# Kernel tuning notes

Measured on AMD Instinct MI355X. Metric: run time of the kernel, lower is better.

The kernel has to match this reference:

```python
import jax, jax.numpy as jnp
import numpy as np

N = 384          # nodes per graph
HID = 128        # hid_dim
H = 8            # shared_num_heads
C = HID // H     # shared_head_dim = 16
L = 4            # num_layers
VOCAB = 20
NORB = 4
NCAT = NORB * NORB + NORB   # 20 edge categories
OUT = 10
B = 4
E = N * N        # fully-connected closure incl. self loops
EPS = 1e-5


def layer_norm(x, g, b):
    m = jnp.mean(x, axis=-1, keepdims=True)
    v = jnp.mean((x - m) ** 2, axis=-1, keepdims=True)
    return (x - m) / jnp.sqrt(v + EPS) * g + b


def setup_inputs() -> dict:
    key = jax.random.key(0)
    ks = iter(jax.random.split(key, 32))

    def nrm(shape, s=0.05):
        return jax.random.normal(next(ks), shape, jnp.float32) * s

    # edge structure: fully connected, edge (i,j) in row-major order
    pos = np.arange(N) % NORB                    # node -> orbit
    src = np.repeat(np.arange(N), N)
    tgt = np.tile(np.arange(N), N)
    cat = np.where(src == tgt, NORB * NORB + pos[src], pos[src] * NORB + pos[tgt])

    x = jax.random.randint(next(ks), (B, N, 1), 0, VOCAB, jnp.int32)

    return dict(
        x=x,
        edge_src=jnp.asarray(src, jnp.int32),
        edge_tgt=jnp.asarray(tgt, jnp.int32),
        edge_cat=jnp.asarray(cat, jnp.int32),
        token_emb=nrm((VOCAB, HID), 1.0),
        edge_emb=nrm((NCAT, HID), 1.0),
        ln_in1_g=jnp.ones((HID,), jnp.float32), ln_in1_b=jnp.zeros((HID,), jnp.float32),
        W_in=nrm((HID, HID)), b_in=jnp.zeros((HID,), jnp.float32),
        ln_in2_g=jnp.ones((HID,), jnp.float32), ln_in2_b=jnp.zeros((HID,), jnp.float32),
        Wl=nrm((L, HID, H * C)), bl=jnp.zeros((L, H * C), jnp.float32),
        Wr=nrm((L, HID, H * C)), br=jnp.zeros((L, H * C), jnp.float32),
        We=nrm((L, HID, H * C)),                           # lin_edge has no bias in PyG GATv2Conv
        att=nrm((L, H, C)),
        bias_gat=jnp.zeros((L, H * C), jnp.float32),
        W_proj=nrm((L, HID, HID)), b_proj=jnp.zeros((L, HID), jnp.float32),
        ln_g=jnp.ones((L, HID), jnp.float32), ln_b=jnp.zeros((L, HID), jnp.float32),
        W_out=nrm((HID, OUT)), b_out=jnp.zeros((OUT,), jnp.float32),
    )


def reference(x, edge_src, edge_tgt, edge_cat,
              token_emb, edge_emb,
              ln_in1_g, ln_in1_b, W_in, b_in, ln_in2_g, ln_in2_b,
              Wl, bl, Wr, br, We, att, bias_gat,
              W_proj, b_proj, ln_g, ln_b, W_out, b_out):
    edge_feat = edge_emb[edge_cat]                       # [E, HID] gather by category
    h = token_emb[x[..., 0]]                             # [B, N, HID]
    # input MLP: LN -> ReLU -> Linear -> LN
    h = layer_norm(h, ln_in1_g, ln_in1_b)
    h = jax.nn.relu(h)
    h = h @ W_in + b_in
    h = layer_norm(h, ln_in2_g, ln_in2_b)

    for l in range(L):
        edge_e = (edge_feat @ We[l]).reshape(E, H, C)    # shared across batch

        def conv(hb):  # hb: [N, HID]  GATv2Conv, concat heads
            xl = (hb @ Wl[l] + bl[l]).reshape(N, H, C)   # source transform
            xr = (hb @ Wr[l] + br[l]).reshape(N, H, C)   # target transform
            e = jax.nn.leaky_relu(xl[edge_src] + xr[edge_tgt] + edge_e, 0.2)  # [E,H,C]
            logits = jnp.einsum('ehc,hc->eh', e, att[l])                      # [E,H]
            # segment softmax over edges sharing a target node
            m = jax.ops.segment_max(logits, edge_tgt, num_segments=N)
            ex = jnp.exp(logits - m[edge_tgt])
            den = jax.ops.segment_sum(ex, edge_tgt, num_segments=N)
            alpha = ex / den[edge_tgt]                                        # [E,H]
            out = jax.ops.segment_sum(xl[edge_src] * alpha[:, :, None], edge_tgt,
                                      num_segments=N)                         # [N,H,C]
            return out.reshape(N, H * C) + bias_gat[l]

        h_prev = h
        h = jax.vmap(conv)(h)                            # [B, N, HID]
        h = h @ W_proj[l] + b_proj[l]
        h = layer_norm(h, ln_g[l], ln_b[l])
        h = jax.nn.relu(h) + h_prev                      # residual

    h = h.sum(axis=1)                                    # sum over nodes -> [B, HID]
    return h @ W_out + b_out                             # [B, OUT]
```

## Files before the change

kernel.cpp:

```cpp
#include <hip/hip_runtime.h>


#define NN 384
#define NB 4
#define TJ 3

__device__ __forceinline__ void reduce32(float& a, float& b) {
#pragma unroll
  for (int m = 1; m <= 16; m <<= 1) {
    a += __shfl_xor(a, m, 64);
    b += __shfl_xor(b, m, 64);
  }
}

__global__ __launch_bounds__(256) void k_init(
    const int* __restrict__ x,
    const float* __restrict__ token_emb, const float* __restrict__ edge_emb,
    const float* __restrict__ ln1g, const float* __restrict__ ln1b,
    const float* __restrict__ W_in, const float* __restrict__ b_in,
    const float* __restrict__ ln2g, const float* __restrict__ ln2b,
    const float* __restrict__ Wl, const float* __restrict__ bl,
    const float* __restrict__ Wr, const float* __restrict__ br,
    const float* __restrict__ We, const float* __restrict__ att_w,
    float* __restrict__ ce, float* __restrict__ h,
    float* __restrict__ xl, float* __restrict__ xr, float* __restrict__ datt0)
{
  const int blk = blockIdx.x, t = threadIdx.x;
  if (blk < 40) {
    const int idx = blk * 256 + t;
    const int hc = idx & 127, rest = idx >> 7;
    const int cat = rest % 20, l = rest / 20;
    const float* er = edge_emb + cat * 128;
    const float* w  = We + (l * 128) * 128 + hc;
    float acc = 0.f;
#pragma unroll 8
    for (int k = 0; k < 128; ++k) acc = fmaf(er[k], w[k * 128], acc);
    ce[idx] = acc;
    return;
  }
  __shared__ float trow[8][128];
  __shared__ float hbuf[8][128];
  const int r0 = (blk - 40) * 8;
  const int r = t >> 5, cw = (t & 31) * 4;
  const int row = r0 + r;
  const int tok = x[row];
  float4 v = *(const float4*)(token_emb + tok * 128 + cw);
  float s1 = v.x + v.y + v.z + v.w;
  float s2 = v.x * v.x + v.y * v.y + v.z * v.z + v.w * v.w;
  reduce32(s1, s2);
  float mean = s1 * 0.0078125f;
  float inv  = rsqrtf(s2 * 0.0078125f - mean * mean + 1e-5f);
  {
    float4 g  = *(const float4*)(ln1g + cw);
    float4 bb = *(const float4*)(ln1b + cw);
    trow[r][cw + 0] = fmaxf((v.x - mean) * inv * g.x + bb.x, 0.f);
    trow[r][cw + 1] = fmaxf((v.y - mean) * inv * g.y + bb.y, 0.f);
    trow[r][cw + 2] = fmaxf((v.z - mean) * inv * g.z + bb.z, 0.f);
    trow[r][cw + 3] = fmaxf((v.w - mean) * inv * g.w + bb.w, 0.f);
  }
  __syncthreads();
  const int o = t & 127, rh = (t >> 7) * 4;
  float a0, a1, a2, a3;
  { float bo = b_in[o]; a0 = a1 = a2 = a3 = bo; }
  for (int k = 0; k < 128; ++k) {
    float w = W_in[k * 128 + o];
    a0 = fmaf(trow[rh + 0][k], w, a0);
    a1 = fmaf(trow[rh + 1][k], w, a1);
    a2 = fmaf(trow[rh + 2][k], w, a2);
    a3 = fmaf(trow[rh + 3][k], w, a3);
  }
  hbuf[rh + 0][o] = a0; hbuf[rh + 1][o] = a1;
  hbuf[rh + 2][o] = a2; hbuf[rh + 3][o] = a3;
  __syncthreads();
  v = *(const float4*)(&hbuf[r][cw]);
  s1 = v.x + v.y + v.z + v.w;
  s2 = v.x * v.x + v.y * v.y + v.z * v.z + v.w * v.w;
  reduce32(s1, s2);
  mean = s1 * 0.0078125f;
  inv  = rsqrtf(s2 * 0.0078125f - mean * mean + 1e-5f);
  {
    float4 g  = *(const float4*)(ln2g + cw);
    float4 bb = *(const float4*)(ln2b + cw);
    float4 hv;
    hv.x = (v.x - mean) * inv * g.x + bb.x;
    hv.y = (v.y - mean) * inv * g.y + bb.y;
    hv.z = (v.z - mean) * inv * g.z + bb.z;
    hv.w = (v.w - mean) * inv * g.w + bb.w;
    *(float4*)(&trow[r][cw]) = hv;
    *(float4*)(h + row * 128 + cw) = hv;
  }
  __syncthreads();
  float l0, l1, l2, l3, q0, q1, q2, q3;
  { float blo = bl[o], bro = br[o]; l0 = l1 = l2 = l3 = blo; q0 = q1 = q2 = q3 = bro; }
  for (int k = 0; k < 128; ++k) {
    float wl = Wl[k * 128 + o], wr = Wr[k * 128 + o];
    float h0 = trow[rh + 0][k], h1 = trow[rh + 1][k];
    float h2 = trow[rh + 2][k], h3 = trow[rh + 3][k];
    l0 = fmaf(h0, wl, l0); q0 = fmaf(h0, wr, q0);
    l1 = fmaf(h1, wl, l1); q1 = fmaf(h1, wr, q1);
    l2 = fmaf(h2, wl, l2); q2 = fmaf(h2, wr, q2);
    l3 = fmaf(h3, wl, l3); q3 = fmaf(h3, wr, q3);
  }
  const int rb = r0 + rh;
  xl[(rb + 0) * 128 + o] = l0; xr[(rb + 0) * 128 + o] = q0;
  xl[(rb + 1) * 128 + o] = l1; xr[(rb + 1) * 128 + o] = q1;
  xl[(rb + 2) * 128 + o] = l2; xr[(rb + 2) * 128 + o] = q2;
  xl[(rb + 3) * 128 + o] = l3; xr[(rb + 3) * 128 + o] = q3;
  {
    float av = att_w[o];
    float s0 = av * l0, sA = av * l1, sB = av * l2, sC = av * l3;
#pragma unroll
    for (int mm = 1; mm <= 8; mm <<= 1) {
      s0 += __shfl_xor(s0, mm, 64);
      sA += __shfl_xor(sA, mm, 64);
      sB += __shfl_xor(sB, mm, 64);
      sC += __shfl_xor(sC, mm, 64);
    }
    if ((t & 15) == 0) {
      const int hh2 = o >> 4;
      const int bb2 = r0 / NN, ii = r0 - bb2 * NN + rh;
      const int base = (bb2 * 8 + hh2) * NN + ii;
      datt0[base + 0] = s0; datt0[base + 1] = sA;
      datt0[base + 2] = sB; datt0[base + 3] = sC;
    }
  }
}

__global__ __launch_bounds__(256) void k_layer(
    const float* __restrict__ xl_in, const float* __restrict__ xr_in,
    const float* __restrict__ datt_in,
    float* __restrict__ xl_out, float* __restrict__ xr_out,
    float* __restrict__ datt_out,
    float* __restrict__ h, const float* __restrict__ ce,
    const float* __restrict__ att_w, const float* __restrict__ bias_gat,
    const float* __restrict__ W_proj, const float* __restrict__ b_proj,
    const float* __restrict__ ln_g, const float* __restrict__ ln_b,
    const float* __restrict__ Wl, const float* __restrict__ bl,
    const float* __restrict__ Wr, const float* __restrict__ br,
    int l, int next_l)
{
  __shared__ float xrce[TJ][5][136];
  __shared__ float djr02[TJ][5][8];
  __shared__ float mbuf[8][32][17];
  __shared__ float arow[TJ][132];
  __shared__ float pbuf[2 * TJ][132];
  __shared__ float nrow[TJ][132];

  const int blk = blockIdx.x, t = threadIdx.x;
  const int jt = blk & 127, b = blk >> 7;
  const int j0 = jt * TJ;

  for (int idx = t; idx < TJ * 5 * 128; idx += 256) {
    const int hc = idx & 127, rest = idx >> 7;
    const int sel = rest % 5, jj = rest / 5;
    const int j = j0 + jj, pj = j & 3;
    const int cat = (sel == 4) ? (16 + pj) : (sel * 4 + pj);
    xrce[jj][sel][hc] = xr_in[(b * NN + j) * 128 + hc] + ce[(l * 20 + cat) * 128 + hc];
  }
  __syncthreads();
  if (t < TJ * 5 * 8) {
    const int jj = t / 40, r2 = t % 40, sel = r2 >> 3, h2 = r2 & 7;
    float d = 0.f;
#pragma unroll
    for (int c = 0; c < 16; ++c)
      d += xrce[jj][sel][h2 * 16 + c] * att_w[l * 128 + h2 * 16 + c];
    djr02[jj][sel][h2] = 0.2f * d;
  }
  __syncthreads();

  const int hh = t >> 5, isub = t & 31;
  float attv[16];
  {
    const float* ap = att_w + l * 128 + hh * 16;
#pragma unroll
    for (int c = 0; c < 16; ++c) attv[c] = ap[c];
  }
  float sden[TJ];
  float acc[TJ][16];
#pragma unroll
  for (int jj = 0; jj < TJ; ++jj) {
    sden[jj] = 0.f;
#pragma unroll
    for (int c = 0; c < 16; ++c) acc[jj][c] = 0.f;
  }
  const float* xlb = xl_in + (b * NN) * 128 + hh * 16;
  const float* dp  = datt_in + (b * 8 + hh) * NN;

  for (int it = 0; it < NN / 32; ++it) {
    const int i = isub + 32 * it;
    float xv[16];
    {
      const float4* xp = (const float4*)(xlb + i * 128);
#pragma unroll
      for (int q = 0; q < 4; ++q) {
        float4 a = xp[q];
        xv[q * 4 + 0] = a.x; xv[q * 4 + 1] = a.y;
        xv[q * 4 + 2] = a.z; xv[q * 4 + 3] = a.w;
      }
    }
    const float di02 = 0.2f * dp[i];
    const int pi = i & 3;
#pragma unroll
    for (int jj = 0; jj < TJ; ++jj) {
      const int sel = (i == j0 + jj) ? 4 : pi;
      const float4* bp = (const float4*)(&xrce[jj][sel][hh * 16]);
      float p = 0.f;
#pragma unroll
      for (int q = 0; q < 4; ++q) {
        float4 cv = bp[q];
        p = fmaf(fmaxf(xv[q * 4 + 0] + cv.x, 0.f), attv[q * 4 + 0], p);
        p = fmaf(fmaxf(xv[q * 4 + 1] + cv.y, 0.f), attv[q * 4 + 1], p);
        p = fmaf(fmaxf(xv[q * 4 + 2] + cv.z, 0.f), attv[q * 4 + 2], p);
        p = fmaf(fmaxf(xv[q * 4 + 3] + cv.w, 0.f), attv[q * 4 + 3], p);
      }
      const float e = __expf(fmaf(0.8f, p, di02 + djr02[jj][sel][hh]));
      sden[jj] += e;
#pragma unroll
      for (int c = 0; c < 16; ++c) acc[jj][c] = fmaf(e, xv[c], acc[jj][c]);
    }
  }

  for (int jj = 0; jj < TJ; ++jj) {
    __syncthreads();
    mbuf[hh][isub][0] = sden[jj];
#pragma unroll
    for (int c = 0; c < 16; ++c) mbuf[hh][isub][1 + c] = acc[jj][c];
    __syncthreads();
    if (t < 128) {
      const int h2 = t >> 4, c2 = t & 15;
      float den = 0.f, num = 0.f;
#pragma unroll 8
      for (int u = 0; u < 32; ++u) {
        den += mbuf[h2][u][0];
        num += mbuf[h2][u][1 + c2];
      }
      arow[jj][t] = num / den + bias_gat[l * 128 + t];
    }
  }
  __syncthreads();

  {
    const int o = t & 127, half = t >> 7;
    const float* Wp = W_proj + l * 16384;
    float p0 = 0.f, p1 = 0.f, p2 = 0.f;
    const int k0 = half * 64;
    for (int kk = 0; kk < 64; ++kk) {
      const int k = k0 + kk;
      const float w = Wp[k * 128 + o];
      p0 = fmaf(arow[0][k], w, p0);
      p1 = fmaf(arow[1][k], w, p1);
      p2 = fmaf(arow[2][k], w, p2);
    }
    pbuf[half * 3 + 0][o] = p0;
    pbuf[half * 3 + 1][o] = p1;
    pbuf[half * 3 + 2][o] = p2;
  }
  __syncthreads();
  if (t < 128) {
    const float bo = b_proj[l * 128 + t];
    nrow[0][t] = pbuf[0][t] + pbuf[3][t] + bo;
    nrow[1][t] = pbuf[1][t] + pbuf[4][t] + bo;
    nrow[2][t] = pbuf[2][t] + pbuf[5][t] + bo;
  }
  __syncthreads();

  {
    const int w = t >> 6;
    if (w < TJ) {
      const int c2 = (t & 63) * 2;
      float v0 = nrow[w][c2], v1 = nrow[w][c2 + 1];
      float s1 = v0 + v1, s2 = v0 * v0 + v1 * v1;
#pragma unroll
      for (int m = 1; m <= 32; m <<= 1) {
        s1 += __shfl_xor(s1, m, 64);
        s2 += __shfl_xor(s2, m, 64);
      }
      const float mean = s1 * 0.0078125f;
      const float inv  = rsqrtf(s2 * 0.0078125f - mean * mean + 1e-5f);
      const int row = (b * NN + j0 + w) * 128;
      const float g0 = ln_g[l * 128 + c2], g1 = ln_g[l * 128 + c2 + 1];
      const float b0 = ln_b[l * 128 + c2], b1 = ln_b[l * 128 + c2 + 1];
      const float hp0 = h[row + c2], hp1 = h[row + c2 + 1];
      const float hn0 = fmaxf((v0 - mean) * inv * g0 + b0, 0.f) + hp0;
      const float hn1 = fmaxf((v1 - mean) * inv * g1 + b1, 0.f) + hp1;
      h[row + c2] = hn0; h[row + c2 + 1] = hn1;
      nrow[w][c2] = hn0; nrow[w][c2 + 1] = hn1;
    }
  }
  __syncthreads();

  if (next_l >= 0) {
    const int o = t & 127, m = t >> 7;
    const float* W = (m ? Wr : Wl) + next_l * 16384;
    const float bias = (m ? br : bl)[next_l * 128 + o];
    float a0 = bias, a1 = bias, a2 = bias;
    for (int k = 0; k < 128; ++k) {
      const float wv = W[k * 128 + o];
      a0 = fmaf(nrow[0][k], wv, a0);
      a1 = fmaf(nrow[1][k], wv, a1);
      a2 = fmaf(nrow[2][k], wv, a2);
    }
    float* dst = m ? xr_out : xl_out;
    const int rb = (b * NN + j0) * 128 + o;
    dst[rb] = a0; dst[rb + 128] = a1; dst[rb + 256] = a2;
    if (m == 0) {
      const float av = att_w[next_l * 128 + o];
      float s0 = av * a0, s1 = av * a1, s2 = av * a2;
#pragma unroll
      for (int mm = 1; mm <= 8; mm <<= 1) {
        s0 += __shfl_xor(s0, mm, 64);
        s1 += __shfl_xor(s1, mm, 64);
        s2 += __shfl_xor(s2, mm, 64);
      }
      if ((t & 15) == 0) {
        const int base = (b * 8 + (o >> 4)) * NN + j0;
        datt_out[base + 0] = s0;
        datt_out[base + 1] = s1;
        datt_out[base + 2] = s2;
      }
    }
  }
}

__global__ __launch_bounds__(256) void k_final(
    const float* __restrict__ h, const float* __restrict__ W_out,
    const float* __restrict__ b_out, float* __restrict__ out)
{
  __shared__ float sbuf[2][128];
  const int bq = blockIdx.x, t = threadIdx.x;
  const int o = t & 127, half = t >> 7;
  float acc = 0.f;
  const float* hp = h + (bq * NN + half * 192) * 128 + o;
  for (int n = 0; n < 192; ++n) acc += hp[n * 128];
  sbuf[half][o] = acc;
  __syncthreads();
  if (t < 10) {
    float a = b_out[t];
#pragma unroll 8
    for (int k = 0; k < 128; ++k)
      a = fmaf(sbuf[0][k] + sbuf[1][k], W_out[k * 10 + t], a);
    out[bq * 10 + t] = a;
  }
}

extern "C" void kernel_launch(void* const* d_in, const int* in_sizes, int n_in,
                              void* d_out, int out_size, void* d_ws, size_t ws_size,
                              hipStream_t stream) {
  const int*   x         = (const int*)d_in[0];
  const float* token_emb = (const float*)d_in[4];
  const float* edge_emb  = (const float*)d_in[5];
  const float* ln1g      = (const float*)d_in[6];
  const float* ln1b      = (const float*)d_in[7];
  const float* W_in      = (const float*)d_in[8];
  const float* b_in      = (const float*)d_in[9];
  const float* ln2g      = (const float*)d_in[10];
  const float* ln2b      = (const float*)d_in[11];
  const float* Wl        = (const float*)d_in[12];
  const float* bl        = (const float*)d_in[13];
  const float* Wr        = (const float*)d_in[14];
  const float* br        = (const float*)d_in[15];
  const float* We        = (const float*)d_in[16];
  const float* att_w     = (const float*)d_in[17];
  const float* bias_gat  = (const float*)d_in[18];
  const float* W_proj    = (const float*)d_in[19];
  const float* b_proj    = (const float*)d_in[20];
  const float* ln_g      = (const float*)d_in[21];
  const float* ln_b      = (const float*)d_in[22];
  const float* W_out     = (const float*)d_in[23];
  const float* b_out     = (const float*)d_in[24];

  float* ws  = (float*)d_ws;
  float* ce  = ws;
  float* h   = ce  + 10240;
  float* xlA = h   + 196608;
  float* xrA = xlA + 196608;
  float* xlB = xrA + 196608;
  float* xrB = xlB + 196608;
  float* dA  = xrB + 196608;
  float* dB  = dA  + 12288;

  k_init<<<dim3(40 + 192), 256, 0, stream>>>(
      x, token_emb, edge_emb, ln1g, ln1b, W_in, b_in, ln2g, ln2b,
      Wl, bl, Wr, br, We, att_w, ce, h, xlA, xrA, dA);
  for (int l = 0; l < 4; ++l) {
    const bool even = (l & 1) == 0;
    float* xin  = even ? xlA : xlB;  float* rin  = even ? xrA : xrB;
    float* din  = even ? dA  : dB;
    float* xout = even ? xlB : xlA;  float* rout = even ? xrB : xrA;
    float* dout = even ? dB  : dA;
    k_layer<<<dim3(NB * (NN / TJ)), 256, 0, stream>>>(
        xin, rin, din, xout, rout, dout, h, ce, att_w, bias_gat,
        W_proj, b_proj, ln_g, ln_b, Wl, bl, Wr, br, l, (l < 3) ? l + 1 : -1);
  }
  k_final<<<dim3(NB), 256, 0, stream>>>(h, W_out, b_out, (float*)d_out);
}
```

Measured before the change: 230.0 us.

## Double k_layer block to 512 threads and split reductions and GEMVs across waves

Raises the k_layer block size from 256 to 512 threads, so each head is now covered by a full 64-lane wave that handles half as many source nodes per thread. The cross-lane reduction is rewritten as a per-wave LDS plus shuffle reduce, which removes the per-jj block barriers. The projection and next-layer GEMVs are split along K across four thread groups with partial sums combined through shared memory. The aim is more parallelism and latency hiding for a grid of only 512 blocks, at the cost of extra shared memory, more barriers in the tail and register pressure under the (512,4) launch bounds.

```diff
diff --git a/kernel.cpp b/kernel.cpp
--- a/kernel.cpp
+++ b/kernel.cpp
@@ -11,6 +11,10 @@
     a += __shfl_xor(a, m, 64);
     b += __shfl_xor(b, m, 64);
   }
+}
+
+__device__ __forceinline__ float uniformf(float x) {
+  return __uint_as_float(__builtin_amdgcn_readfirstlane(__float_as_uint(x)));
 }
 
 __global__ __launch_bounds__(256) void k_init(
@@ -126,7 +130,7 @@
   }
 }
 
-__global__ __launch_bounds__(256) void k_layer(
+__global__ __launch_bounds__(512, 4) void k_layer(
     const float* __restrict__ xl_in, const float* __restrict__ xr_in,
     const float* __restrict__ datt_in,
     float* __restrict__ xl_out, float* __restrict__ xr_out,
@@ -141,16 +145,16 @@
 {
   __shared__ float xrce[TJ][5][136];
   __shared__ float djr02[TJ][5][8];
-  __shared__ float mbuf[8][32][17];
+  __shared__ float mbuf[8][64][17];
   __shared__ float arow[TJ][132];
-  __shared__ float pbuf[2 * TJ][132];
+  __shared__ float pbuf[12][132];
   __shared__ float nrow[TJ][132];
 
   const int blk = blockIdx.x, t = threadIdx.x;
   const int jt = blk & 127, b = blk >> 7;
   const int j0 = jt * TJ;
 
-  for (int idx = t; idx < TJ * 5 * 128; idx += 256) {
+  for (int idx = t; idx < TJ * 5 * 128; idx += 512) {
     const int hc = idx & 127, rest = idx >> 7;
     const int sel = rest % 5, jj = rest / 5;
     const int j = j0 + jj, pj = j & 3;
@@ -168,12 +172,12 @@
   }
   __syncthreads();
 
-  const int hh = t >> 5, isub = t & 31;
+  const int hh = t >> 6, isub = t & 63;
   float attv[16];
   {
     const float* ap = att_w + l * 128 + hh * 16;
 #pragma unroll
-    for (int c = 0; c < 16; ++c) attv[c] = ap[c];
+    for (int c = 0; c < 16; ++c) attv[c] = uniformf(ap[c]);
   }
   float sden[TJ];
   float acc[TJ][16];
@@ -186,8 +190,9 @@
   const float* xlb = xl_in + (b * NN) * 128 + hh * 16;
   const float* dp  = datt_in + (b * 8 + hh) * NN;
 
-  for (int it = 0; it < NN / 32; ++it) {
-    const int i = isub + 32 * it;
+#pragma unroll 2
+  for (int it = 0; it < NN / 64; ++it) {
+    const int i = isub + 64 * it;
     float xv[16];
     {
       const float4* xp = (const float4*)(xlb + i * 128);
@@ -220,47 +225,49 @@
     }
   }
 
-  for (int jj = 0; jj < TJ; ++jj) {
-    __syncthreads();
-    mbuf[hh][isub][0] = sden[jj];
-#pragma unroll
-    for (int c = 0; c < 16; ++c) mbuf[hh][isub][1 + c] = acc[jj][c];
-    __syncthreads();
-    if (t < 128) {
-      const int h2 = t >> 4, c2 = t & 15;
-      float den = 0.f, num = 0.f;
-#pragma unroll 8
-      for (int u = 0; u < 32; ++u) {
-        den += mbuf[h2][u][0];
-        num += mbuf[h2][u][1 + c2];
-      }
-      arow[jj][t] = num / den + bias_gat[l * 128 + t];
-    }
-  }
-  __syncthreads();
-
-  {
-    const int o = t & 127, half = t >> 7;
+  {
+    const int lc = isub & 15, up = isub >> 4;
+#pragma unroll
+    for (int jj = 0; jj < TJ; ++jj) {
+      mbuf[hh][isub][0] = sden[jj];
+#pragma unroll
+      for (int c = 0; c < 16; ++c) mbuf[hh][isub][1 + c] = acc[jj][c];
+      float nsum = 0.f, dsum = 0.f;
+#pragma unroll 4
+      for (int u2 = 0; u2 < 16; ++u2) {
+        const int u = up * 16 + u2;
+        dsum += mbuf[hh][u][0];
+        nsum += mbuf[hh][u][1 + lc];
+      }
+      nsum += __shfl_xor(nsum, 16, 64); dsum += __shfl_xor(dsum, 16, 64);
+      nsum += __shfl_xor(nsum, 32, 64); dsum += __shfl_xor(dsum, 32, 64);
+      if (isub < 16)
+        arow[jj][hh * 16 + isub] = nsum / dsum + bias_gat[l * 128 + hh * 16 + isub];
+    }
+  }
+  __syncthreads();
+
+  {
+    const int o = t & 127, g = t >> 7;
     const float* Wp = W_proj + l * 16384;
     float p0 = 0.f, p1 = 0.f, p2 = 0.f;
-    const int k0 = half * 64;
-    for (int kk = 0; kk < 64; ++kk) {
+    const int k0 = g * 32;
+    for (int kk = 0; kk < 32; ++kk) {
       const int k = k0 + kk;
       const float w = Wp[k * 128 + o];
       p0 = fmaf(arow[0][k], w, p0);
       p1 = fmaf(arow[1][k], w, p1);
       p2 = fmaf(arow[2][k], w, p2);
     }
-    pbuf[half * 3 + 0][o] = p0;
-    pbuf[half * 3 + 1][o] = p1;
-    pbuf[half * 3 + 2][o] = p2;
-  }
-  __syncthreads();
-  if (t < 128) {
-    const float bo = b_proj[l * 128 + t];
-    nrow[0][t] = pbuf[0][t] + pbuf[3][t] + bo;
-    nrow[1][t] = pbuf[1][t] + pbuf[4][t] + bo;
-    nrow[2][t] = pbuf[2][t] + pbuf[5][t] + bo;
+    pbuf[g * 3 + 0][o] = p0;
+    pbuf[g * 3 + 1][o] = p1;
+    pbuf[g * 3 + 2][o] = p2;
+  }
+  __syncthreads();
+  if (t < 384) {
+    const int rr = t >> 7, o = t & 127;
+    nrow[rr][o] = pbuf[rr][o] + pbuf[3 + rr][o] + pbuf[6 + rr][o] + pbuf[9 + rr][o]
+                + b_proj[l * 128 + o];
   }
   __syncthreads();
 
@@ -290,22 +297,34 @@
   __syncthreads();
 
   if (next_l >= 0) {
-    const int o = t & 127, m = t >> 7;
-    const float* W = (m ? Wr : Wl) + next_l * 16384;
-    const float bias = (m ? br : bl)[next_l * 128 + o];
-    float a0 = bias, a1 = bias, a2 = bias;
-    for (int k = 0; k < 128; ++k) {
+    const int o = t & 127, g = t >> 7;
+    const float* W = ((g & 2) ? Wr : Wl) + next_l * 16384;
+    const int k0 = (g & 1) * 64;
+    float a0 = 0.f, a1 = 0.f, a2 = 0.f;
+    for (int kk = 0; kk < 64; ++kk) {
+      const int k = k0 + kk;
       const float wv = W[k * 128 + o];
       a0 = fmaf(nrow[0][k], wv, a0);
       a1 = fmaf(nrow[1][k], wv, a1);
       a2 = fmaf(nrow[2][k], wv, a2);
     }
-    float* dst = m ? xr_out : xl_out;
-    const int rb = (b * NN + j0) * 128 + o;
-    dst[rb] = a0; dst[rb + 128] = a1; dst[rb + 256] = a2;
-    if (m == 0) {
-      const float av = att_w[next_l * 128 + o];
-      float s0 = av * a0, s1 = av * a1, s2 = av * a2;
+    pbuf[g * 3 + 0][o] = a0;
+    pbuf[g * 3 + 1][o] = a1;
+    pbuf[g * 3 + 2][o] = a2;
+    __syncthreads();
+    for (int idx = t; idx < 768; idx += 512) {
+      const int m = idx / 384;
+      const int rr = (idx - m * 384) >> 7, o2 = idx & 127;
+      const float bias = (m ? br : bl)[next_l * 128 + o2];
+      const float v = pbuf[m * 6 + rr][o2] + pbuf[m * 6 + 3 + rr][o2] + bias;
+      float* dst = m ? xr_out : xl_out;
+      dst[(b * NN + j0 + rr) * 128 + o2] = v;
+      if (m == 0) arow[rr][o2] = v;
+    }
+    __syncthreads();
+    if (t < 128) {
+      const float av = att_w[next_l * 128 + t];
+      float s0 = av * arow[0][t], s1 = av * arow[1][t], s2 = av * arow[2][t];
 #pragma unroll
       for (int mm = 1; mm <= 8; mm <<= 1) {
         s0 += __shfl_xor(s0, mm, 64);
@@ -313,7 +332,7 @@
         s2 += __shfl_xor(s2, mm, 64);
       }
       if ((t & 15) == 0) {
-        const int base = (b * 8 + (o >> 4)) * NN + j0;
+        const int base = (b * 8 + (t >> 4)) * NN + j0;
         datt_out[base + 0] = s0;
         datt_out[base + 1] = s1;
         datt_out[base + 2] = s2;
@@ -388,7 +407,7 @@
     float* din  = even ? dA  : dB;
     float* xout = even ? xlB : xlA;  float* rout = even ? xrB : xrA;
     float* dout = even ? dB  : dA;
-    k_layer<<<dim3(NB * (NN / TJ)), 256, 0, stream>>>(
+    k_layer<<<dim3(NB * (NN / TJ)), 512, 0, stream>>>(
         xin, rin, din, xout, rout, dout, h, ce, att_w, bias_gat,
         W_proj, b_proj, ln_g, ln_b, Wl, bl, Wr, br, l, (l < 3) ? l + 1 : -1);
   }
```

After: 221.4 us. 1.04x faster.

## Shrink target tile to two nodes, hoist per-thread edge-category terms, warp-local reduction

Applied to the files above, without the earlier changes.

The layer kernel now handles two target nodes per block instead of three, which doubles the grid to 768 blocks over a 2D launch. Because each thread's source index keeps a fixed residue mod 4, the per-category xr+ce vectors are hoisted into registers and the diagonal self-loop case becomes a rare branch. The cross-lane reduction of numerators and denominators is done within each wave, removing the block barriers inside that loop. The init kernel is retiled to four rows per block with separate Wl/Wr halves. The aim is more parallelism and less LDS traffic, at the cost of more blocks and weight reloads per block.

```diff
diff --git a/kernel.cpp b/kernel.cpp
--- a/kernel.cpp
+++ b/kernel.cpp
@@ -3,11 +3,11 @@
 
 #define NN 384
 #define NB 4
-#define TJ 3
-
-__device__ __forceinline__ void reduce32(float& a, float& b) {
-#pragma unroll
-  for (int m = 1; m <= 16; m <<= 1) {
+#define TJ 2
+
+__device__ __forceinline__ void reduce64(float& a, float& b) {
+#pragma unroll
+  for (int m = 1; m <= 32; m <<= 1) {
     a += __shfl_xor(a, m, 64);
     b += __shfl_xor(b, m, 64);
   }
@@ -38,77 +38,72 @@
     ce[idx] = acc;
     return;
   }
-  __shared__ float trow[8][128];
-  __shared__ float hbuf[8][128];
-  const int r0 = (blk - 40) * 8;
-  const int r = t >> 5, cw = (t & 31) * 4;
+  __shared__ float trow[4][128];
+  __shared__ float hbuf[4][128];
+  const int r0 = (blk - 40) * 4;
+  const int r = t >> 6, c2 = (t & 63) * 2;
   const int row = r0 + r;
   const int tok = x[row];
-  float4 v = *(const float4*)(token_emb + tok * 128 + cw);
-  float s1 = v.x + v.y + v.z + v.w;
-  float s2 = v.x * v.x + v.y * v.y + v.z * v.z + v.w * v.w;
-  reduce32(s1, s2);
+  float2 v = *(const float2*)(token_emb + tok * 128 + c2);
+  float s1 = v.x + v.y;
+  float s2 = v.x * v.x + v.y * v.y;
+  reduce64(s1, s2);
   float mean = s1 * 0.0078125f;
   float inv  = rsqrtf(s2 * 0.0078125f - mean * mean + 1e-5f);
   {
-    float4 g  = *(const float4*)(ln1g + cw);
-    float4 bb = *(const float4*)(ln1b + cw);
-    trow[r][cw + 0] = fmaxf((v.x - mean) * inv * g.x + bb.x, 0.f);
-    trow[r][cw + 1] = fmaxf((v.y - mean) * inv * g.y + bb.y, 0.f);
-    trow[r][cw + 2] = fmaxf((v.z - mean) * inv * g.z + bb.z, 0.f);
-    trow[r][cw + 3] = fmaxf((v.w - mean) * inv * g.w + bb.w, 0.f);
-  }
-  __syncthreads();
-  const int o = t & 127, rh = (t >> 7) * 4;
-  float a0, a1, a2, a3;
-  { float bo = b_in[o]; a0 = a1 = a2 = a3 = bo; }
-  for (int k = 0; k < 128; ++k) {
-    float w = W_in[k * 128 + o];
-    a0 = fmaf(trow[rh + 0][k], w, a0);
-    a1 = fmaf(trow[rh + 1][k], w, a1);
-    a2 = fmaf(trow[rh + 2][k], w, a2);
-    a3 = fmaf(trow[rh + 3][k], w, a3);
-  }
-  hbuf[rh + 0][o] = a0; hbuf[rh + 1][o] = a1;
-  hbuf[rh + 2][o] = a2; hbuf[rh + 3][o] = a3;
-  __syncthreads();
-  v = *(const float4*)(&hbuf[r][cw]);
-  s1 = v.x + v.y + v.z + v.w;
-  s2 = v.x * v.x + v.y * v.y + v.z * v.z + v.w * v.w;
-  reduce32(s1, s2);
+    float2 g  = *(const float2*)(ln1g + c2);
+    float2 bb = *(const float2*)(ln1b + c2);
+    trow[r][c2 + 0] = fmaxf((v.x - mean) * inv * g.x + bb.x, 0.f);
+    trow[r][c2 + 1] = fmaxf((v.y - mean) * inv * g.y + bb.y, 0.f);
+  }
+  __syncthreads();
+  const int o = t & 127, rh = (t >> 7) * 2;
+  {
+    float a0, a1;
+    { float bo = b_in[o]; a0 = a1 = bo; }
+    for (int k = 0; k < 128; ++k) {
+      float w = W_in[k * 128 + o];
+      a0 = fmaf(trow[rh + 0][k], w, a0);
+      a1 = fmaf(trow[rh + 1][k], w, a1);
+    }
+    hbuf[rh + 0][o] = a0; hbuf[rh + 1][o] = a1;
+  }
+  __syncthreads();
+  v = *(const float2*)(&hbuf[r][c2]);
+  s1 = v.x + v.y;
+  s2 = v.x * v.x + v.y * v.y;
+  reduce64(s1, s2);
   mean = s1 * 0.0078125f;
   inv  = rsqrtf(s2 * 0.0078125f - mean * mean + 1e-5f);
   {
-    float4 g  = *(const float4*)(ln2g + cw);
-    float4 bb = *(const float4*)(ln2b + cw);
-    float4 hv;
+    float2 g  = *(const float2*)(ln2g + c2);
+    float2 bb = *(const float2*)(ln2b + c2);
+    float2 hv;
     hv.x = (v.x - mean) * inv * g.x + bb.x;
     hv.y = (v.y - mean) * inv * g.y + bb.y;
-    hv.z = (v.z - mean) * inv * g.z + bb.z;
-    hv.w = (v.w - mean) * inv * g.w + bb.w;
-    *(float4*)(&trow[r][cw]) = hv;
-    *(float4*)(h + row * 128 + cw) = hv;
-  }
-  __syncthreads();
-  float l0, l1, l2, l3, q0, q1, q2, q3;
-  { float blo = bl[o], bro = br[o]; l0 = l1 = l2 = l3 = blo; q0 = q1 = q2 = q3 = bro; }
+    trow[r][c2] = hv.x; trow[r][c2 + 1] = hv.y;
+    *(float2*)(h + row * 128 + c2) = hv;
+  }
+  __syncthreads();
+  const int m = t >> 7;
+  const float* W = m ? Wr : Wl;
+  const float bias = (m ? br : bl)[o];
+  float a0 = bias, a1 = bias, a2 = bias, a3 = bias;
   for (int k = 0; k < 128; ++k) {
-    float wl = Wl[k * 128 + o], wr = Wr[k * 128 + o];
-    float h0 = trow[rh + 0][k], h1 = trow[rh + 1][k];
-    float h2 = trow[rh + 2][k], h3 = trow[rh + 3][k];
-    l0 = fmaf(h0, wl, l0); q0 = fmaf(h0, wr, q0);
-    l1 = fmaf(h1, wl, l1); q1 = fmaf(h1, wr, q1);
-    l2 = fmaf(h2, wl, l2); q2 = fmaf(h2, wr, q2);
-    l3 = fmaf(h3, wl, l3); q3 = fmaf(h3, wr, q3);
-  }
-  const int rb = r0 + rh;
-  xl[(rb + 0) * 128 + o] = l0; xr[(rb + 0) * 128 + o] = q0;
-  xl[(rb + 1) * 128 + o] = l1; xr[(rb + 1) * 128 + o] = q1;
-  xl[(rb + 2) * 128 + o] = l2; xr[(rb + 2) * 128 + o] = q2;
-  xl[(rb + 3) * 128 + o] = l3; xr[(rb + 3) * 128 + o] = q3;
-  {
+    float wv = W[k * 128 + o];
+    a0 = fmaf(trow[0][k], wv, a0);
+    a1 = fmaf(trow[1][k], wv, a1);
+    a2 = fmaf(trow[2][k], wv, a2);
+    a3 = fmaf(trow[3][k], wv, a3);
+  }
+  float* dst = m ? xr : xl;
+  dst[(r0 + 0) * 128 + o] = a0;
+  dst[(r0 + 1) * 128 + o] = a1;
+  dst[(r0 + 2) * 128 + o] = a2;
+  dst[(r0 + 3) * 128 + o] = a3;
+  if (m == 0) {
     float av = att_w[o];
-    float s0 = av * l0, sA = av * l1, sB = av * l2, sC = av * l3;
+    float s0 = av * a0, sA = av * a1, sB = av * a2, sC = av * a3;
 #pragma unroll
     for (int mm = 1; mm <= 8; mm <<= 1) {
       s0 += __shfl_xor(s0, mm, 64);
@@ -118,8 +113,8 @@
     }
     if ((t & 15) == 0) {
       const int hh2 = o >> 4;
-      const int bb2 = r0 / NN, ii = r0 - bb2 * NN + rh;
-      const int base = (bb2 * 8 + hh2) * NN + ii;
+      const int b2 = r0 / NN, ii = r0 - b2 * NN;
+      const int base = (b2 * 8 + hh2) * NN + ii;
       datt0[base + 0] = s0; datt0[base + 1] = sA;
       datt0[base + 2] = sB; datt0[base + 3] = sC;
     }
@@ -146,8 +141,8 @@
   __shared__ float pbuf[2 * TJ][132];
   __shared__ float nrow[TJ][132];
 
-  const int blk = blockIdx.x, t = threadIdx.x;
-  const int jt = blk & 127, b = blk >> 7;
+  const int t = threadIdx.x;
+  const int jt = blockIdx.x, b = blockIdx.y;
   const int j0 = jt * TJ;
 
   for (int idx = t; idx < TJ * 5 * 128; idx += 256) {
@@ -155,7 +150,8 @@
     const int sel = rest % 5, jj = rest / 5;
     const int j = j0 + jj, pj = j & 3;
     const int cat = (sel == 4) ? (16 + pj) : (sel * 4 + pj);
-    xrce[jj][sel][hc] = xr_in[(b * NN + j) * 128 + hc] + ce[(l * 20 + cat) * 128 + hc];
+    xrce[jj][sel][hc] = xr_in[(b * NN + j) * 128 + hc]
+                      + ce[(l * 20 + cat) * 128 + hc];
   }
   __syncthreads();
   if (t < TJ * 5 * 8) {
@@ -175,6 +171,19 @@
 #pragma unroll
     for (int c = 0; c < 16; ++c) attv[c] = ap[c];
   }
+  const int pfix = isub & 3;
+  float cvj[TJ][16], djf[TJ];
+#pragma unroll
+  for (int jj = 0; jj < TJ; ++jj) {
+    const float4* cp = (const float4*)(&xrce[jj][pfix][hh * 16]);
+#pragma unroll
+    for (int q = 0; q < 4; ++q) {
+      float4 cv = cp[q];
+      cvj[jj][q * 4 + 0] = cv.x; cvj[jj][q * 4 + 1] = cv.y;
+      cvj[jj][q * 4 + 2] = cv.z; cvj[jj][q * 4 + 3] = cv.w;
+    }
+    djf[jj] = djr02[jj][pfix][hh];
+  }
   float sden[TJ];
   float acc[TJ][16];
 #pragma unroll
@@ -186,6 +195,7 @@
   const float* xlb = xl_in + (b * NN) * 128 + hh * 16;
   const float* dp  = datt_in + (b * 8 + hh) * NN;
 
+#pragma unroll 2
   for (int it = 0; it < NN / 32; ++it) {
     const int i = isub + 32 * it;
     float xv[16];
@@ -199,68 +209,69 @@
       }
     }
     const float di02 = 0.2f * dp[i];
-    const int pi = i & 3;
 #pragma unroll
     for (int jj = 0; jj < TJ; ++jj) {
-      const int sel = (i == j0 + jj) ? 4 : pi;
-      const float4* bp = (const float4*)(&xrce[jj][sel][hh * 16]);
       float p = 0.f;
 #pragma unroll
-      for (int q = 0; q < 4; ++q) {
-        float4 cv = bp[q];
-        p = fmaf(fmaxf(xv[q * 4 + 0] + cv.x, 0.f), attv[q * 4 + 0], p);
-        p = fmaf(fmaxf(xv[q * 4 + 1] + cv.y, 0.f), attv[q * 4 + 1], p);
-        p = fmaf(fmaxf(xv[q * 4 + 2] + cv.z, 0.f), attv[q * 4 + 2], p);
-        p = fmaf(fmaxf(xv[q * 4 + 3] + cv.w, 0.f), attv[q * 4 + 3], p);
-      }
-      const float e = __expf(fmaf(0.8f, p, di02 + djr02[jj][sel][hh]));
+      for (int c = 0; c < 16; ++c)
+        p = fmaf(fmaxf(xv[c] + cvj[jj][c], 0.f), attv[c], p);
+      float dj = djf[jj];
+      if (i == j0 + jj) {
+        const float* b4 = &xrce[jj][4][hh * 16];
+        float ps = 0.f;
+#pragma unroll
+        for (int c = 0; c < 16; ++c)
+          ps = fmaf(fmaxf(xv[c] + b4[c], 0.f), attv[c], ps);
+        p = ps;
+        dj = djr02[jj][4][hh];
+      }
+      const float e = __expf(fmaf(0.8f, p, di02 + dj));
       sden[jj] += e;
 #pragma unroll
       for (int c = 0; c < 16; ++c) acc[jj][c] = fmaf(e, xv[c], acc[jj][c]);
     }
   }
 
-  for (int jj = 0; jj < TJ; ++jj) {
-    __syncthreads();
-    mbuf[hh][isub][0] = sden[jj];
-#pragma unroll
-    for (int c = 0; c < 16; ++c) mbuf[hh][isub][1 + c] = acc[jj][c];
-    __syncthreads();
-    if (t < 128) {
-      const int h2 = t >> 4, c2 = t & 15;
-      float den = 0.f, num = 0.f;
-#pragma unroll 8
-      for (int u = 0; u < 32; ++u) {
-        den += mbuf[h2][u][0];
-        num += mbuf[h2][u][1 + c2];
-      }
-      arow[jj][t] = num / den + bias_gat[l * 128 + t];
-    }
-  }
-  __syncthreads();
-
-  {
-    const int o = t & 127, half = t >> 7;
+  {
+    const int lc = isub & 15, up = isub >> 4;
+#pragma unroll
+    for (int jj = 0; jj < TJ; ++jj) {
+      mbuf[hh][isub][0] = sden[jj];
+#pragma unroll
+      for (int c = 0; c < 16; ++c) mbuf[hh][isub][1 + c] = acc[jj][c];
+      float nsum = 0.f, dsum = 0.f;
+#pragma unroll 4
+      for (int u2 = 0; u2 < 16; ++u2) {
+        const int u = up * 16 + u2;
+        dsum += mbuf[hh][u][0];
+        nsum += mbuf[hh][u][1 + lc];
+      }
+      nsum += __shfl_xor(nsum, 16, 64); dsum += __shfl_xor(dsum, 16, 64);
+      if (isub < 16)
+        arow[jj][hh * 16 + isub] =
+            nsum / dsum + bias_gat[l * 128 + hh * 16 + isub];
+    }
+  }
+  __syncthreads();
+
+  {
+    const int o = t & 127, g4 = t >> 7;
     const float* Wp = W_proj + l * 16384;
-    float p0 = 0.f, p1 = 0.f, p2 = 0.f;
-    const int k0 = half * 64;
+    float p0 = 0.f, p1 = 0.f;
+    const int k0 = g4 * 64;
     for (int kk = 0; kk < 64; ++kk) {
       const int k = k0 + kk;
       const float w = Wp[k * 128 + o];
       p0 = fmaf(arow[0][k], w, p0);
       p1 = fmaf(arow[1][k], w, p1);
-      p2 = fmaf(arow[2][k], w, p2);
-    }
-    pbuf[half * 3 + 0][o] = p0;
-    pbuf[half * 3 + 1][o] = p1;
-    pbuf[half * 3 + 2][o] = p2;
-  }
-  __syncthreads();
-  if (t < 128) {
-    const float bo = b_proj[l * 128 + t];
-    nrow[0][t] = pbuf[0][t] + pbuf[3][t] + bo;
-    nrow[1][t] = pbuf[1][t] + pbuf[4][t] + bo;
-    nrow[2][t] = pbuf[2][t] + pbuf[5][t] + bo;
+    }
+    pbuf[g4 * 2 + 0][o] = p0;
+    pbuf[g4 * 2 + 1][o] = p1;
+  }
+  __syncthreads();
+  {
+    const int rr = t >> 7, o = t & 127;
+    nrow[rr][o] = pbuf[rr][o] + pbuf[2 + rr][o] + b_proj[l * 128 + o];
   }
   __syncthreads();
 
@@ -293,30 +304,27 @@
     const int o = t & 127, m = t >> 7;
     const float* W = (m ? Wr : Wl) + next_l * 16384;
     const float bias = (m ? br : bl)[next_l * 128 + o];
-    float a0 = bias, a1 = bias, a2 = bias;
+    float a0 = bias, a1 = bias;
     for (int k = 0; k < 128; ++k) {
       const float wv = W[k * 128 + o];
       a0 = fmaf(nrow[0][k], wv, a0);
       a1 = fmaf(nrow[1][k], wv, a1);
-      a2 = fmaf(nrow[2][k], wv, a2);
     }
     float* dst = m ? xr_out : xl_out;
     const int rb = (b * NN + j0) * 128 + o;
-    dst[rb] = a0; dst[rb + 128] = a1; dst[rb + 256] = a2;
+    dst[rb] = a0; dst[rb + 128] = a1;
     if (m == 0) {
       const float av = att_w[next_l * 128 + o];
-      float s0 = av * a0, s1 = av * a1, s2 = av * a2;
+      float s0 = av * a0, s1 = av * a1;
 #pragma unroll
       for (int mm = 1; mm <= 8; mm <<= 1) {
         s0 += __shfl_xor(s0, mm, 64);
         s1 += __shfl_xor(s1, mm, 64);
-        s2 += __shfl_xor(s2, mm, 64);
       }
       if ((t & 15) == 0) {
         const int base = (b * 8 + (o >> 4)) * NN + j0;
         datt_out[base + 0] = s0;
         datt_out[base + 1] = s1;
-        datt_out[base + 2] = s2;
       }
     }
   }
@@ -379,7 +387,7 @@
   float* dA  = xrB + 196608;
   float* dB  = dA  + 12288;
 
-  k_init<<<dim3(40 + 192), 256, 0, stream>>>(
+  k_init<<<dim3(40 + 384), 256, 0, stream>>>(
       x, token_emb, edge_emb, ln1g, ln1b, W_in, b_in, ln2g, ln2b,
       Wl, bl, Wr, br, We, att_w, ce, h, xlA, xrA, dA);
   for (int l = 0; l < 4; ++l) {
@@ -388,7 +396,7 @@
     float* din  = even ? dA  : dB;
     float* xout = even ? xlB : xlA;  float* rout = even ? xrB : xrA;
     float* dout = even ? dB  : dA;
-    k_layer<<<dim3(NB * (NN / TJ)), 256, 0, stream>>>(
+    k_layer<<<dim3(NN / TJ, NB), 256, 0, stream>>>(
         xin, rin, din, xout, rout, dout, h, ce, att_w, bias_gat,
         W_proj, b_proj, ln_g, ln_b, Wl, bl, Wr, br, l, (l < 3) ? l + 1 : -1);
   }
```

New measurement: 237.5 us. +3.2%, slower.
